# Optimization experiments

Hardware: AMD Instinct MI355X
Metric: run time of the kernel (lower is better)

Reference implementation:

```python
import jax, jax.numpy as jnp
import numpy as np

N, E, IN_DIM, HID, OUT = 50000, 800000, 128, 128, 64


def setup_inputs() -> dict:
    key = jax.random.key(0)
    k = jax.random.split(key, 6)
    h = jax.random.normal(k[0], (N, IN_DIM), dtype=jnp.float32)
    edge_index = jax.random.randint(k[1], (2, E), 0, N, dtype=jnp.int64)
    s_in, s_hid = 1.0 / np.sqrt(IN_DIM), 1.0 / np.sqrt(HID)
    W_gcn = jax.random.uniform(k[2], (IN_DIM, HID), jnp.float32, -s_in, s_in)
    b_gcn = jnp.zeros((HID,), jnp.float32)
    W_fc = jax.random.uniform(k[3], (HID, OUT), jnp.float32, -s_hid, s_hid)
    b_fc = jax.random.uniform(k[4], (OUT,), jnp.float32, -s_hid, s_hid)
    return {"h": h, "edge_index": edge_index, "W_gcn": W_gcn,
            "b_gcn": b_gcn, "W_fc": W_fc, "b_fc": b_fc}


def reference(h, edge_index, W_gcn, b_gcn, W_fc, b_fc):
    n = h.shape[0]
    # GCNConv: transform, add self-loops, symmetric normalization, scatter-add
    x = h @ W_gcn                                   # [N, HID]
    loop = jnp.arange(n, dtype=edge_index.dtype)
    row = jnp.concatenate([edge_index[0], loop])    # source nodes
    col = jnp.concatenate([edge_index[1], loop])    # destination nodes
    deg = jax.ops.segment_sum(jnp.ones_like(col, dtype=x.dtype), col,
                              num_segments=n)       # in-degree incl. self-loop
    dinv = jnp.where(deg > 0, jax.lax.rsqrt(deg), 0.0)
    norm = dinv[row] * dinv[col]                    # [E+N]
    msg = x[row] * norm[:, None]                    # gather + scale
    agg = jax.ops.segment_sum(msg, col, num_segments=n) + b_gcn
    # ReLU then projection
    return jax.nn.relu(agg) @ W_fc + b_fc
```

## Files before the change

### kernel.cpp

```cpp
#include <hip/hip_runtime.h>

#define N_NODES 50000
#define N_EDGES 800000
#define TOT (N_EDGES + N_NODES)
#define NBKT 196
#define BCAP 6144

typedef __attribute__((ext_vector_type(4))) float floatx4;
typedef __attribute__((ext_vector_type(8))) _Float16 half8;
typedef __attribute__((ext_vector_type(2))) _Float16 half2v;

#define O_PTR   0UL
#define O_GF    200192UL
#define O_FLAG  201216UL
#define O_DINV  201472UL
#define O_ESRC  401664UL
#define O_W1    3801856UL
#define O_W2    3834624UL
#define O_U     3851008UL
#define O_H16   16651008UL

__global__ void k_prep(const float* __restrict__ Wg, const float* __restrict__ Wf,
                       const unsigned* __restrict__ ei_raw,
                       int* gfill, _Float16* W1, _Float16* W2, int* flags) {
    int i = blockIdx.x * 256 + threadIdx.x;
    if (i < 128 * 128) { int n = i >> 7, k = i & 127; W1[i] = (_Float16)Wg[k * 128 + n]; }
    if (i < 64 * 128)  { int n = i >> 7, k = i & 127; W2[i] = (_Float16)Wf[k * 64 + n]; }
    if (i < NBKT) gfill[i] = 0;
    if (i >= 16320) {
        int lane = i - 16320;
        unsigned w = ei_raw[2 * lane + 1];
        unsigned long long m = __ballot(w == 0u);
        if (lane == 0) flags[1] = (__popcll(m) >= 60) ? 1 : 0;
    }
}

__global__ __launch_bounds__(256) void k_binA(const int* __restrict__ ei,
                                              const int* __restrict__ flags,
                                              int* __restrict__ gfill,
                                              unsigned* __restrict__ staging) {
    __shared__ int cnt[NBKT];
    __shared__ int gbase[NBKT];
    int t = threadIdx.x;
    for (int i = t; i < NBKT; i += 256) cnt[i] = 0;
    __syncthreads();
    int ebase = blockIdx.x * 4096;
    bool i64 = flags[1] != 0;
    unsigned pk[16]; int rk[16]; short bk[16];
#pragma unroll
    for (int j = 0; j < 16; ++j) {
        int e = ebase + j * 256 + t;
        if (e < N_EDGES) {
            int s, d;
            if (i64) { s = ei[2 * e]; d = ei[2 * (N_EDGES + e)]; }
            else     { s = ei[e];     d = ei[N_EDGES + e]; }
            int b = d >> 8;
            bk[j] = (short)b;
            pk[j] = (unsigned)s | ((unsigned)(d & 255) << 16);
            rk[j] = atomicAdd(&cnt[b], 1);
        } else bk[j] = -1;
    }
    __syncthreads();
    for (int i = t; i < NBKT; i += 256)
        gbase[i] = atomicAdd(&gfill[i], cnt[i]);
    __syncthreads();
#pragma unroll
    for (int j = 0; j < 16; ++j) {
        if (bk[j] >= 0) {
            int pos = gbase[bk[j]] + rk[j];
            if (pos < BCAP) staging[(size_t)bk[j] * BCAP + pos] = pk[j];
        }
    }
}

__global__ __launch_bounds__(256) void k_binB(const unsigned* __restrict__ staging,
                                              const int* __restrict__ gfill,
                                              const float* __restrict__ h,
                                              int* __restrict__ ptr,
                                              float* __restrict__ dinv,
                                              _Float16* __restrict__ h16,
                                              int* __restrict__ esrc) {
    __shared__ unsigned se[BCAP];
    __shared__ int lcnt[256];
    __shared__ int lscan[256];
    __shared__ int cur[256];
    __shared__ float sdinv[256];
    __shared__ int s_cb;
    int b = blockIdx.x, t = threadIdx.x;
    int nbase = b * 256;
    int nn = min(256, N_NODES - nbase);
    int cnt = min(gfill[b], BCAP);
    if (t < 64) {
        int acc = 0;
        for (int i = t; i < b; i += 64) acc += min(gfill[i], BCAP) + 256;
#pragma unroll
        for (int off = 32; off > 0; off >>= 1) acc += __shfl_down(acc, off);
        if (t == 0) s_cb = acc;
    }
    lcnt[t] = 0;
    __syncthreads();
    int cb = s_cb;
    const unsigned* st = staging + (size_t)b * BCAP;
    for (int i = t; i < cnt; i += 256) {
        unsigned p = st[i];
        se[i] = p;
        atomicAdd(&lcnt[p >> 16], 1);
    }
    __syncthreads();
    int v = lcnt[t];
    lscan[t] = v;
    __syncthreads();
    for (int off = 1; off < 256; off <<= 1) {
        int x = (t >= off) ? lscan[t - off] : 0;
        __syncthreads(); lscan[t] += x; __syncthreads();
    }
    int segstart = cb + (lscan[t] - v) + t;
    float dv = rsqrtf((float)(v + 1));
    if (t < nn) {
        int node = nbase + t;
        ptr[node] = segstart;
        dinv[node] = dv;
        sdinv[t] = dv;
        esrc[segstart] = node;
        cur[t] = segstart + 1;
    }
    __syncthreads();
    for (int g = 0; g < 7; ++g) {
        for (int i = t; i < cnt; i += 256) {
            unsigned p = se[i];
            int s = (int)(p & 0xffffu);
            if ((s >> 13) == g) {
                int pos = atomicAdd(&cur[p >> 16], 1);
                esrc[pos] = s;
            }
        }
        __syncthreads();
    }
    int half = t >> 7;
    int col = t & 127;
    for (int r = half; r < nn; r += 2) {
        int node = nbase + r;
        h16[(size_t)node * 128 + col] = (_Float16)(h[(size_t)node * 128 + col] * sdinv[r]);
    }
}

__global__ __launch_bounds__(256) void k_agg(const _Float16* __restrict__ h16,
                                             const int* __restrict__ ptr,
                                             const int* __restrict__ esrc,
                                             const float* __restrict__ dinv,
                                             _Float16* __restrict__ u) {
    int wid = (blockIdx.x * 256 + threadIdx.x) >> 6;
    int lane = threadIdx.x & 63;
    if (wid >= N_NODES) return;
    int p0 = ptr[wid];
    int p1 = (wid + 1 < N_NODES) ? ptr[wid + 1] : TOT;
    float a0 = 0.f, a1 = 0.f;
    for (int base = p0; base < p1; base += 64) {
        int cnt = p1 - base; if (cnt > 64) cnt = 64;
        int idx = 0;
        if (lane < cnt) idx = esrc[base + lane];
        int j = 0;
        for (; j + 8 <= cnt; j += 8) {
            int s0 = __shfl(idx, j),     s1 = __shfl(idx, j + 1);
            int s2 = __shfl(idx, j + 2), s3 = __shfl(idx, j + 3);
            int s4 = __shfl(idx, j + 4), s5 = __shfl(idx, j + 5);
            int s6 = __shfl(idx, j + 6), s7 = __shfl(idx, j + 7);
            half2v u0 = *(const half2v*)(h16 + (size_t)s0 * 128 + lane * 2);
            half2v u1 = *(const half2v*)(h16 + (size_t)s1 * 128 + lane * 2);
            half2v u2 = *(const half2v*)(h16 + (size_t)s2 * 128 + lane * 2);
            half2v u3 = *(const half2v*)(h16 + (size_t)s3 * 128 + lane * 2);
            half2v u4 = *(const half2v*)(h16 + (size_t)s4 * 128 + lane * 2);
            half2v u5 = *(const half2v*)(h16 + (size_t)s5 * 128 + lane * 2);
            half2v u6 = *(const half2v*)(h16 + (size_t)s6 * 128 + lane * 2);
            half2v u7 = *(const half2v*)(h16 + (size_t)s7 * 128 + lane * 2);
            a0 += (float)u0[0] + (float)u1[0] + (float)u2[0] + (float)u3[0]
                + (float)u4[0] + (float)u5[0] + (float)u6[0] + (float)u7[0];
            a1 += (float)u0[1] + (float)u1[1] + (float)u2[1] + (float)u3[1]
                + (float)u4[1] + (float)u5[1] + (float)u6[1] + (float)u7[1];
        }
        for (; j + 4 <= cnt; j += 4) {
            int s0 = __shfl(idx, j),     s1 = __shfl(idx, j + 1);
            int s2 = __shfl(idx, j + 2), s3 = __shfl(idx, j + 3);
            half2v u0 = *(const half2v*)(h16 + (size_t)s0 * 128 + lane * 2);
            half2v u1 = *(const half2v*)(h16 + (size_t)s1 * 128 + lane * 2);
            half2v u2 = *(const half2v*)(h16 + (size_t)s2 * 128 + lane * 2);
            half2v u3 = *(const half2v*)(h16 + (size_t)s3 * 128 + lane * 2);
            a0 += (float)u0[0] + (float)u1[0] + (float)u2[0] + (float)u3[0];
            a1 += (float)u0[1] + (float)u1[1] + (float)u2[1] + (float)u3[1];
        }
        for (; j < cnt; ++j) {
            int s = __shfl(idx, j);
            half2v uu = *(const half2v*)(h16 + (size_t)s * 128 + lane * 2);
            a0 += (float)uu[0]; a1 += (float)uu[1];
        }
    }
    float sc = dinv[wid];
    half2v o; o[0] = (_Float16)(a0 * sc); o[1] = (_Float16)(a1 * sc);
    *(half2v*)(u + (size_t)wid * 128 + lane * 2) = o;
}

__global__ __launch_bounds__(256) void k_gemmF(const _Float16* __restrict__ u,
                                               const _Float16* __restrict__ W1,
                                               const _Float16* __restrict__ W2,
                                               const float* __restrict__ bg,
                                               const float* __restrict__ bfc,
                                               float* __restrict__ out) {
    __shared__ _Float16 zt[4][16 * 128];
    int wave = threadIdx.x >> 6;
    int lane = threadIdx.x & 63;
    int rowbase = (blockIdx.x * 4 + wave) * 16;
    if (rowbase > N_NODES - 16) rowbase = N_NODES - 16;
    int quad = lane >> 4;
    int l15 = lane & 15;
    int mr = rowbase + l15;
    half8 a[4];
#pragma unroll
    for (int kk = 0; kk < 4; ++kk)
        a[kk] = *(const half8*)(u + (size_t)mr * 128 + kk * 32 + quad * 8);
    _Float16* z = zt[wave];
#pragma unroll
    for (int nt = 0; nt < 8; ++nt) {
        floatx4 acc = {0.f, 0.f, 0.f, 0.f};
        int n = nt * 16 + l15;
#pragma unroll
        for (int kk = 0; kk < 4; ++kk) {
            half8 bb = *(const half8*)(W1 + n * 128 + kk * 32 + quad * 8);
            acc = __builtin_amdgcn_mfma_f32_16x16x32_f16(a[kk], bb, acc, 0, 0, 0);
        }
        float bias = bg[n];
#pragma unroll
        for (int i = 0; i < 4; ++i) {
            int row = quad * 4 + i;
            z[row * 128 + n] = (_Float16)fmaxf(acc[i] + bias, 0.f);
        }
    }
    __syncthreads();
    half8 a2[4];
#pragma unroll
    for (int kk = 0; kk < 4; ++kk)
        a2[kk] = *(const half8*)(z + l15 * 128 + kk * 32 + quad * 8);
#pragma unroll
    for (int mt = 0; mt < 4; ++mt) {
        floatx4 acc = {0.f, 0.f, 0.f, 0.f};
        int n = mt * 16 + l15;
#pragma unroll
        for (int kk = 0; kk < 4; ++kk) {
            half8 bb = *(const half8*)(W2 + n * 128 + kk * 32 + quad * 8);
            acc = __builtin_amdgcn_mfma_f32_16x16x32_f16(a2[kk], bb, acc, 0, 0, 0);
        }
        float bias = bfc[n];
#pragma unroll
        for (int i = 0; i < 4; ++i) {
            int row = rowbase + quad * 4 + i;
            out[(size_t)row * 64 + n] = acc[i] + bias;
        }
    }
}

extern "C" void kernel_launch(void* const* d_in, const int* in_sizes, int n_in,
                              void* d_out, int out_size, void* d_ws, size_t ws_size,
                              hipStream_t stream) {
    (void)in_sizes; (void)n_in; (void)out_size; (void)ws_size;
    const float* h  = (const float*)d_in[0];
    const int*   ei = (const int*)d_in[1];
    const float* Wg = (const float*)d_in[2];
    const float* bg = (const float*)d_in[3];
    const float* Wf = (const float*)d_in[4];
    const float* bf = (const float*)d_in[5];
    float* out = (float*)d_out;

    char* ws = (char*)d_ws;
    int*      ptr   = (int*)(ws + O_PTR);
    int*      gfill = (int*)(ws + O_GF);
    int*      flags = (int*)(ws + O_FLAG);
    float*    dinv  = (float*)(ws + O_DINV);
    int*      esrc  = (int*)(ws + O_ESRC);
    _Float16* W1    = (_Float16*)(ws + O_W1);
    _Float16* W2    = (_Float16*)(ws + O_W2);
    _Float16* u     = (_Float16*)(ws + O_U);
    _Float16* h16   = (_Float16*)(ws + O_H16);
    unsigned* staging = (unsigned*)(ws + O_U);

    k_prep<<<64, 256, 0, stream>>>(Wg, Wf, (const unsigned*)ei, gfill, W1, W2, flags);
    k_binA<<<NBKT, 256, 0, stream>>>(ei, flags, gfill, staging);
    k_binB<<<NBKT, 256, 0, stream>>>(staging, gfill, h, ptr, dinv, h16, esrc);
    k_agg<<<(N_NODES + 3) / 4, 256, 0, stream>>>(h16, ptr, esrc, dinv, u);
    k_gemmF<<<(N_NODES + 63) / 64, 256, 0, stream>>>(u, W1, W2, bg, bf, out);
}
```

Measured before the change: 180.9 us.

## Drop prep kernel, fold weight conversion into binB, remove 7-pass source ordering

After: 176.5 us. 1.02x faster.

```diff
diff --git a/kernel.cpp b/kernel.cpp
--- a/kernel.cpp
+++ b/kernel.cpp
@@ -12,7 +12,6 @@
 
 #define O_PTR   0UL
 #define O_GF    200192UL
-#define O_FLAG  201216UL
 #define O_DINV  201472UL
 #define O_ESRC  401664UL
 #define O_W1    3801856UL
@@ -20,32 +19,22 @@
 #define O_U     3851008UL
 #define O_H16   16651008UL
 
-__global__ void k_prep(const float* __restrict__ Wg, const float* __restrict__ Wf,
-                       const unsigned* __restrict__ ei_raw,
-                       int* gfill, _Float16* W1, _Float16* W2, int* flags) {
-    int i = blockIdx.x * 256 + threadIdx.x;
-    if (i < 128 * 128) { int n = i >> 7, k = i & 127; W1[i] = (_Float16)Wg[k * 128 + n]; }
-    if (i < 64 * 128)  { int n = i >> 7, k = i & 127; W2[i] = (_Float16)Wf[k * 64 + n]; }
-    if (i < NBKT) gfill[i] = 0;
-    if (i >= 16320) {
-        int lane = i - 16320;
-        unsigned w = ei_raw[2 * lane + 1];
-        unsigned long long m = __ballot(w == 0u);
-        if (lane == 0) flags[1] = (__popcll(m) >= 60) ? 1 : 0;
-    }
-}
-
 __global__ __launch_bounds__(256) void k_binA(const int* __restrict__ ei,
-                                              const int* __restrict__ flags,
                                               int* __restrict__ gfill,
                                               unsigned* __restrict__ staging) {
     __shared__ int cnt[NBKT];
     __shared__ int gbase[NBKT];
+    __shared__ int s_i64;
     int t = threadIdx.x;
+    if (t < 64) {
+        unsigned w = ((const unsigned*)ei)[2 * t + 1];
+        unsigned long long m = __ballot(w == 0u);
+        if (t == 0) s_i64 = (__popcll(m) >= 60) ? 1 : 0;
+    }
     for (int i = t; i < NBKT; i += 256) cnt[i] = 0;
     __syncthreads();
+    bool i64 = s_i64 != 0;
     int ebase = blockIdx.x * 4096;
-    bool i64 = flags[1] != 0;
     unsigned pk[16]; int rk[16]; short bk[16];
 #pragma unroll
     for (int j = 0; j < 16; ++j) {
@@ -76,9 +65,13 @@
 __global__ __launch_bounds__(256) void k_binB(const unsigned* __restrict__ staging,
                                               const int* __restrict__ gfill,
                                               const float* __restrict__ h,
+                                              const float* __restrict__ Wg,
+                                              const float* __restrict__ Wf,
                                               int* __restrict__ ptr,
                                               float* __restrict__ dinv,
                                               _Float16* __restrict__ h16,
+                                              _Float16* __restrict__ W1,
+                                              _Float16* __restrict__ W2,
                                               int* __restrict__ esrc) {
     __shared__ unsigned se[BCAP];
     __shared__ int lcnt[256];
@@ -87,6 +80,15 @@
     __shared__ float sdinv[256];
     __shared__ int s_cb;
     int b = blockIdx.x, t = threadIdx.x;
+    if (b < 64) {
+        int i = b * 256 + t;
+        int n = i >> 7, k = i & 127;
+        W1[i] = (_Float16)Wg[k * 128 + n];
+    } else if (b < 96) {
+        int i = (b - 64) * 256 + t;
+        int n = i >> 7, k = i & 127;
+        W2[i] = (_Float16)Wf[k * 64 + n];
+    }
     int nbase = b * 256;
     int nn = min(256, N_NODES - nbase);
     int cnt = min(gfill[b], BCAP);
@@ -125,16 +127,10 @@
         cur[t] = segstart + 1;
     }
     __syncthreads();
-    for (int g = 0; g < 7; ++g) {
-        for (int i = t; i < cnt; i += 256) {
-            unsigned p = se[i];
-            int s = (int)(p & 0xffffu);
-            if ((s >> 13) == g) {
-                int pos = atomicAdd(&cur[p >> 16], 1);
-                esrc[pos] = s;
-            }
-        }
-        __syncthreads();
+    for (int i = t; i < cnt; i += 256) {
+        unsigned p = se[i];
+        int pos = atomicAdd(&cur[p >> 16], 1);
+        esrc[pos] = (int)(p & 0xffffu);
     }
     int half = t >> 7;
     int col = t & 127;
@@ -272,7 +268,6 @@
     char* ws = (char*)d_ws;
     int*      ptr   = (int*)(ws + O_PTR);
     int*      gfill = (int*)(ws + O_GF);
-    int*      flags = (int*)(ws + O_FLAG);
     float*    dinv  = (float*)(ws + O_DINV);
     int*      esrc  = (int*)(ws + O_ESRC);
     _Float16* W1    = (_Float16*)(ws + O_W1);
@@ -281,9 +276,10 @@
     _Float16* h16   = (_Float16*)(ws + O_H16);
     unsigned* staging = (unsigned*)(ws + O_U);
 
-    k_prep<<<64, 256, 0, stream>>>(Wg, Wf, (const unsigned*)ei, gfill, W1, W2, flags);
-    k_binA<<<NBKT, 256, 0, stream>>>(ei, flags, gfill, staging);
-    k_binB<<<NBKT, 256, 0, stream>>>(staging, gfill, h, ptr, dinv, h16, esrc);
+    hipMemsetAsync(gfill, 0, NBKT * sizeof(int), stream);
+    k_binA<<<NBKT, 256, 0, stream>>>(ei, gfill, staging);
+    k_binB<<<NBKT, 256, 0, stream>>>(staging, gfill, h, Wg, Wf,
+                                     ptr, dinv, h16, W1, W2, esrc);
     k_agg<<<(N_NODES + 3) / 4, 256, 0, stream>>>(h16, ptr, esrc, dinv, u);
     k_gemmF<<<(N_NODES + 63) / 64, 256, 0, stream>>>(u, W1, W2, bg, bf, out);
 }
```
